# Optimization experiments

Hardware: AMD Instinct MI355X
Metric: run time of the kernel (lower is better)

## Reference

```python
import jax, jax.numpy as jnp
import numpy as np

N = 100000
E = 1600000
NFEAT = 256
NHID = 128
LATENT = 64


def setup_inputs() -> dict:
    key = jax.random.key(0)
    ks = jax.random.split(key, 12)
    x = jax.random.normal(ks[0], (N, NFEAT), dtype=jnp.float32)
    edge_index = jax.random.randint(ks[1], (2, E), 0, N, dtype=jnp.int32)
    edge_weight = jax.random.uniform(ks[2], (E,), dtype=jnp.float32)
    # GraphConvolution params: uniform(-stdv, stdv), stdv = 1/sqrt(out_features)
    s1 = 1.0 / np.sqrt(NHID)
    gc1_w = jax.random.uniform(ks[3], (NFEAT, NHID), minval=-s1, maxval=s1, dtype=jnp.float32)
    gc1_b = jax.random.uniform(ks[4], (NHID,), minval=-s1, maxval=s1, dtype=jnp.float32)
    gc2_w = jax.random.uniform(ks[5], (NHID, NHID), minval=-s1, maxval=s1, dtype=jnp.float32)
    gc2_b = jax.random.uniform(ks[6], (NHID,), minval=-s1, maxval=s1, dtype=jnp.float32)
    # nn.Linear default init: uniform(-1/sqrt(fan_in), 1/sqrt(fan_in))
    s2 = 1.0 / np.sqrt(NHID)
    mu_w = jax.random.uniform(ks[7], (NHID, LATENT), minval=-s2, maxval=s2, dtype=jnp.float32)
    mu_b = jax.random.uniform(ks[8], (LATENT,), minval=-s2, maxval=s2, dtype=jnp.float32)
    lv_w = jax.random.uniform(ks[9], (NHID, LATENT), minval=-s2, maxval=s2, dtype=jnp.float32)
    lv_b = jax.random.uniform(ks[10], (LATENT,), minval=-s2, maxval=s2, dtype=jnp.float32)
    return {"x": x, "edge_index": edge_index, "edge_weight": edge_weight,
            "gc1_w": gc1_w, "gc1_b": gc1_b, "gc2_w": gc2_w, "gc2_b": gc2_b,
            "mu_w": mu_w, "mu_b": mu_b, "lv_w": lv_w, "lv_b": lv_b}


def _spmm(edge_index, edge_weight, support):
    # out[row] += w * support[col]  (sparse adj @ dense support)
    row, col = edge_index[0], edge_index[1]
    msgs = support[col] * edge_weight[:, None]          # [E, F]
    return jax.ops.segment_sum(msgs, row, num_segments=N)


def reference(x, edge_index, edge_weight, gc1_w, gc1_b, gc2_w, gc2_b,
              mu_w, mu_b, lv_w, lv_b):
    # gc1: mm -> spmm -> bias -> relu (dropout is identity in eval mode)
    h = jax.nn.relu(_spmm(edge_index, edge_weight, x @ gc1_w) + gc1_b)
    h = jax.nn.relu(_spmm(edge_index, edge_weight, h @ gc2_w) + gc2_b)
    mu = h @ mu_w + mu_b
    log_var = h @ lv_w + lv_b
    return mu, log_var
```

## Files before the change

kernel.cpp:

```cpp
#include <hip/hip_runtime.h>
#include <hip/hip_fp16.h>

#define N_NODES 100000
#define N_EDGES 1600000
#define NFEAT   256
#define NHID    128
#define LATENT  64

#define NBUCKET 782
#define NBLKH   196
#define CHUNK   8192
#define NHIST   (NBUCKET * NBLKH)
#define NHISTT  300

typedef __attribute__((ext_vector_type(8))) short s16x8;
typedef __attribute__((ext_vector_type(4))) float f32x4;

__device__ __forceinline__ unsigned short f2bf(float f) {
    union { float f; unsigned u; } v; v.f = f;
    unsigned r = v.u + 0x7fffu + ((v.u >> 16) & 1u);
    return (unsigned short)(r >> 16);
}
__device__ __forceinline__ float bf2f(unsigned short s) {
    union { unsigned u; float f; } v; v.u = ((unsigned)s) << 16;
    return v.f;
}
__device__ __forceinline__ float bflo(unsigned u) {
    union { unsigned x; float f; } v; v.x = u << 16; return v.f;
}
__device__ __forceinline__ float bfhi(unsigned u) {
    union { unsigned x; float f; } v; v.x = u & 0xffff0000u; return v.f;
}
__device__ __forceinline__ float w15_decode(unsigned pv) {
    return __half2float(__ushort_as_half((unsigned short)(pv & 0x7fffu)));
}

__device__ __forceinline__ int incl_scan512(int v, int t, int (&s)[2][512]) {
    s[0][t] = v;
    __syncthreads();
    int p = 0;
    for (int off = 1; off < 512; off <<= 1) {
        int x = s[p][t];
        if (t >= off) x += s[p][t - off];
        s[p ^ 1][t] = x;
        p ^= 1;
        __syncthreads();
    }
    return s[p][t];
}


__device__ __forceinline__ void prep_body(
    int c, int K, int Ntot, int ncol0, int ldb0, int ldb1,
    const float* __restrict__ B0, const float* __restrict__ B1,
    unsigned short* __restrict__ out)
{
    int K8 = K >> 3;
    int total = (Ntot >> 4) * K8 * 16;
    if (c >= total) return;
    int m  = c & 15;
    int kc = (c >> 4) % K8;
    int nt = (c >> 4) / K8;
    int col = nt * 16 + m;
    const float* src; int ld, cc;
    if (col < ncol0) { src = B0; ld = ldb0; cc = col; }
    else             { src = B1; ld = ldb1; cc = col - ncol0; }
    s16x8 v;
    #pragma unroll
    for (int j = 0; j < 8; ++j)
        v[j] = (short)f2bf(src[(size_t)(kc * 8 + j) * ld + cc]);
    *(s16x8*)&out[(size_t)c * 8] = v;
}


__global__ __launch_bounds__(256) void k_pre(
    const int* __restrict__ rows, int* __restrict__ histG,
    const float* __restrict__ gc1_w, unsigned short* __restrict__ w1p,
    const float* __restrict__ gc2_w, unsigned short* __restrict__ w2p,
    const float* __restrict__ mu_w, const float* __restrict__ lv_w,
    unsigned short* __restrict__ w3p)
{
    int b = blockIdx.x;
    int t = threadIdx.x;
    if (b < NBLKH) {
        __shared__ int hist[NBUCKET];
        for (int i = t; i < NBUCKET; i += 256) hist[i] = 0;
        __syncthreads();
        int base = b * CHUNK;
        #pragma unroll 4
        for (int i = 0; i < CHUNK / 256; ++i) {
            int e = base + i * 256 + t;
            if (e < N_EDGES) {
                int r = rows[e];
                atomicAdd(&hist[r >> 7], 1);
            }
        }
        __syncthreads();
        for (int i = t; i < NBUCKET; i += 256)
            histG[(size_t)i * NBLKH + b] = hist[i];
    } else if (b < NBLKH + 16) {
        prep_body((b - NBLKH) * 256 + t, NFEAT, NHID, NHID, NHID, NHID, gc1_w, gc1_w, w1p);
    } else if (b < NBLKH + 24) {
        prep_body((b - NBLKH - 16) * 256 + t, NHID, NHID, NHID, NHID, NHID, gc2_w, gc2_w, w2p);
    } else {
        prep_body((b - NBLKH - 24) * 256 + t, NHID, NHID, LATENT, LATENT, LATENT, mu_w, lv_w, w3p);
    }
}


__global__ __launch_bounds__(512) void k_scanA(
    const int* __restrict__ histG, int* __restrict__ hist_excl,
    int* __restrict__ hbsum)
{
    __shared__ int s[2][512];
    int b = blockIdx.x, t = threadIdx.x;
    int i = b * 512 + t;
    int v = (i < NHIST) ? histG[i] : 0;
    int incl = incl_scan512(v, t, s);
    if (i < NHIST) hist_excl[i] = incl - v;
    if (t == 511) hbsum[b] = incl;
}

__global__ __launch_bounds__(512) void k_scanC(
    const int* __restrict__ hist_excl, const int* __restrict__ hbsum,
    int* __restrict__ scanned)
{
    __shared__ int s[2][512];
    __shared__ int sbase;
    int b = blockIdx.x, t = threadIdx.x;
    int v = (t < NHISTT) ? hbsum[t] : 0;
    int incl = incl_scan512(v, t, s);
    if (t == b) sbase = incl - v;
    __syncthreads();
    int base = sbase;
    int i = b * 512 + t;
    if (i < NHIST) scanned[i] = hist_excl[i] + base;
}


__global__ __launch_bounds__(256) void k_scatterA(
    const int* __restrict__ rows, const int* __restrict__ cols,
    const float* __restrict__ ew, const int* __restrict__ scanned,
    uint2* __restrict__ tmp)
{
    __shared__ int cur[NBUCKET];
    int b = blockIdx.x, t = threadIdx.x;
    for (int i = t; i < NBUCKET; i += 256)
        cur[i] = scanned[(size_t)i * NBLKH + b];
    __syncthreads();
    int base = b * CHUNK;
    #pragma unroll 4
    for (int i = 0; i < CHUNK / 256; ++i) {
        int e = base + i * 256 + t;
        if (e < N_EDGES) {
            int r = rows[e];
            unsigned hv = (unsigned)__half_as_ushort(__float2half(ew[e]));
            unsigned pv = ((unsigned)cols[e] << 15) | (hv & 0x7fffu);
            int p = atomicAdd(&cur[r >> 7], 1);
            tmp[p] = make_uint2(pv, (unsigned)r);
        }
    }
}


__global__ __launch_bounds__(256) void k_passB(
    const int* __restrict__ scanned, const uint2* __restrict__ tmp,
    unsigned* __restrict__ ecw, int* __restrict__ row_ptr)
{
    __shared__ int cnt[128];
    __shared__ int sc[2][128];
    __shared__ int cur[128];
    int b  = blockIdx.x;
    int t  = threadIdx.x;
    int r0 = b * 128;
    int beg = scanned[(size_t)b * NBLKH];
    int end = (b + 1 < NBUCKET) ? scanned[(size_t)(b + 1) * NBLKH] : N_EDGES;
    if (t < 128) cnt[t] = 0;
    __syncthreads();
    for (int e = beg + t; e < end; e += 256)
        atomicAdd(&cnt[tmp[e].y & 127], 1);
    __syncthreads();
    int p = 0;
    if (t < 128) sc[0][t] = cnt[t];
    __syncthreads();
    for (int off = 1; off < 128; off <<= 1) {
        if (t < 128) {
            int x = sc[p][t];
            if (t >= off) x += sc[p][t - off];
            sc[p ^ 1][t] = x;
        }
        p ^= 1;
        __syncthreads();
    }
    if (t < 128) {
        int excl = sc[p][t] - cnt[t];
        int rr = r0 + t;
        if (rr < N_NODES) row_ptr[rr] = beg + excl;
        cur[t] = beg + excl;
    }
    if (b == NBUCKET - 1 && t == 0) row_ptr[N_NODES] = N_EDGES;
    __syncthreads();
    for (int e = beg + t; e < end; e += 256) {
        uint2 v = tmp[e];
        int pos = atomicAdd(&cur[v.y & 127], 1);
        ecw[pos] = v.x;
    }
}


template<int AMODE, int OMODE>
__global__ __launch_bounds__(256) void k_gemm(
    int K, const float* __restrict__ A32, const unsigned short* __restrict__ A16,
    const unsigned short* __restrict__ Bpre,
    unsigned short* __restrict__ C16,
    float* __restrict__ C0, float* __restrict__ C1,
    const float* __restrict__ bias0, const float* __restrict__ bias1)
{
    __shared__ unsigned short As[2048];
    __shared__ unsigned short Bs[8192];

    const int t    = threadIdx.x;
    const int m0   = blockIdx.x * 32;
    const int lane = t & 63;
    const int w    = t >> 6;
    const int rt   = w & 1;
    const int ntb  = (w >> 1) * 4;
    const int fm   = lane & 15;
    const int q    = lane >> 4;
    const int K8   = K >> 3;

    f32x4 acc[4] = {};

    for (int kt = 0; kt < K; kt += 64) {
        {
            int r = t >> 3, kc = t & 7;
            int lo = ((r >> 4) * 8 + kc) * 128 + (r & 15) * 8;
            if (AMODE == 0) {
                const float* g = A32 + (size_t)(m0 + r) * K + kt + kc * 8;
                float4 a = *(const float4*)g;
                float4 b = *(const float4*)(g + 4);
                s16x8 v;
                v[0] = (short)f2bf(a.x); v[1] = (short)f2bf(a.y);
                v[2] = (short)f2bf(a.z); v[3] = (short)f2bf(a.w);
                v[4] = (short)f2bf(b.x); v[5] = (short)f2bf(b.y);
                v[6] = (short)f2bf(b.z); v[7] = (short)f2bf(b.w);
                *(s16x8*)&As[lo] = v;
            } else {
                const unsigned short* g = A16 + (size_t)(m0 + r) * 128 + kt + kc * 8;
                *(s16x8*)&As[lo] = *(const s16x8*)g;
            }
        }
        {
            int ktc = kt >> 3;
            #pragma unroll
            for (int i = 0; i < 4; ++i) {
                int c  = t + i * 256;
                int nt = c >> 7, kc = (c >> 4) & 7, m = c & 15;
                const unsigned short* g =
                    Bpre + ((size_t)(nt * K8 + ktc + kc) * 16 + m) * 8;
                *(s16x8*)&Bs[c * 8] = *(const s16x8*)g;
            }
        }
        __syncthreads();
        #pragma unroll
        for (int kk = 0; kk < 2; ++kk) {
            int kcq = kk * 4 + q;
            s16x8 a = *(const s16x8*)&As[(rt * 8 + kcq) * 128 + fm * 8];
            #pragma unroll
            for (int i = 0; i < 4; ++i) {
                s16x8 b = *(const s16x8*)&Bs[((ntb + i) * 8 + kcq) * 128 + fm * 8];
                acc[i] = __builtin_amdgcn_mfma_f32_16x16x32_bf16(a, b, acc[i], 0, 0, 0);
            }
        }
        __syncthreads();
    }

    #pragma unroll
    for (int i = 0; i < 4; ++i) {
        int col = (ntb + i) * 16 + fm;
        #pragma unroll
        for (int j = 0; j < 4; ++j) {
            int r = m0 + rt * 16 + q * 4 + j;
            float v = acc[i][j];
            if (OMODE == 0) {
                C16[(size_t)r * 128 + col] = f2bf(v);
            } else {
                if (col < 64) C0[(size_t)r * 64 + col]      = v + bias0[col];
                else          C1[(size_t)r * 64 + col - 64] = v + bias1[col - 64];
            }
        }
    }
}


#define EDGE4(qq, vv, aa0, aa1, aa2, aa3)                \
    {                                                    \
        float ww = w15_decode(qq);                       \
        aa0 += ww * bflo(vv.x);                          \
        aa1 += ww * bfhi(vv.x);                          \
        aa2 += ww * bflo(vv.y);                          \
        aa3 += ww * bfhi(vv.y);                          \
    }

__global__ __launch_bounds__(256) void k_spmm(const int* __restrict__ row_ptr,
                                              const unsigned* __restrict__ ecw,
                                              const unsigned short* __restrict__ sup,
                                              const float* __restrict__ bias,
                                              unsigned short* __restrict__ out) {
    int wave = threadIdx.x >> 6;
    int lane = threadIdx.x & 63;
    int row  = blockIdx.x * 4 + wave;
    if (row >= N_NODES) return;
    int half = lane >> 5;
    int fl   = lane & 31;

    int beg = row_ptr[row];
    int end = row_ptr[row + 1];
    float a0 = 0.f, a1 = 0.f, a2 = 0.f, a3 = 0.f;
    float b0 = 0.f, b1 = 0.f, b2 = 0.f, b3 = 0.f;

    int e = beg;
    for (; e + 16 <= end; e += 16) {
        unsigned q0 = ecw[e + 0 + half];
        unsigned q1 = ecw[e + 2 + half];
        unsigned q2 = ecw[e + 4 + half];
        unsigned q3 = ecw[e + 6 + half];
        unsigned q4 = ecw[e + 8 + half];
        unsigned q5 = ecw[e + 10 + half];
        unsigned q6 = ecw[e + 12 + half];
        unsigned q7 = ecw[e + 14 + half];
        uint2 v0 = *(const uint2*)(sup + (size_t)(q0 >> 15) * NHID + fl * 4);
        uint2 v1 = *(const uint2*)(sup + (size_t)(q1 >> 15) * NHID + fl * 4);
        uint2 v2 = *(const uint2*)(sup + (size_t)(q2 >> 15) * NHID + fl * 4);
        uint2 v3 = *(const uint2*)(sup + (size_t)(q3 >> 15) * NHID + fl * 4);
        uint2 v4 = *(const uint2*)(sup + (size_t)(q4 >> 15) * NHID + fl * 4);
        uint2 v5 = *(const uint2*)(sup + (size_t)(q5 >> 15) * NHID + fl * 4);
        uint2 v6 = *(const uint2*)(sup + (size_t)(q6 >> 15) * NHID + fl * 4);
        uint2 v7 = *(const uint2*)(sup + (size_t)(q7 >> 15) * NHID + fl * 4);
        EDGE4(q0, v0, a0, a1, a2, a3)
        EDGE4(q1, v1, b0, b1, b2, b3)
        EDGE4(q2, v2, a0, a1, a2, a3)
        EDGE4(q3, v3, b0, b1, b2, b3)
        EDGE4(q4, v4, a0, a1, a2, a3)
        EDGE4(q5, v5, b0, b1, b2, b3)
        EDGE4(q6, v6, a0, a1, a2, a3)
        EDGE4(q7, v7, b0, b1, b2, b3)
    }
    for (; e + 8 <= end; e += 8) {
        unsigned q0 = ecw[e + 0 + half];
        unsigned q1 = ecw[e + 2 + half];
        unsigned q2 = ecw[e + 4 + half];
        unsigned q3 = ecw[e + 6 + half];
        uint2 v0 = *(const uint2*)(sup + (size_t)(q0 >> 15) * NHID + fl * 4);
        uint2 v1 = *(const uint2*)(sup + (size_t)(q1 >> 15) * NHID + fl * 4);
        uint2 v2 = *(const uint2*)(sup + (size_t)(q2 >> 15) * NHID + fl * 4);
        uint2 v3 = *(const uint2*)(sup + (size_t)(q3 >> 15) * NHID + fl * 4);
        EDGE4(q0, v0, a0, a1, a2, a3)
        EDGE4(q1, v1, b0, b1, b2, b3)
        EDGE4(q2, v2, a0, a1, a2, a3)
        EDGE4(q3, v3, b0, b1, b2, b3)
    }
    if (e < end) {
        int last = end - 1;
        int e0 = e + 0 + half, e1 = e + 2 + half;
        int e2 = e + 4 + half, e3 = e + 6 + half;
        unsigned q0 = ecw[e0 <= last ? e0 : last];
        unsigned q1 = ecw[e1 <= last ? e1 : last];
        unsigned q2 = ecw[e2 <= last ? e2 : last];
        unsigned q3 = ecw[e3 <= last ? e3 : last];
        uint2 v0 = *(const uint2*)(sup + (size_t)(q0 >> 15) * NHID + fl * 4);
        uint2 v1 = *(const uint2*)(sup + (size_t)(q1 >> 15) * NHID + fl * 4);
        uint2 v2 = *(const uint2*)(sup + (size_t)(q2 >> 15) * NHID + fl * 4);
        uint2 v3 = *(const uint2*)(sup + (size_t)(q3 >> 15) * NHID + fl * 4);
        float w0 = (e0 <= last) ? w15_decode(q0) : 0.f;
        float w1 = (e1 <= last) ? w15_decode(q1) : 0.f;
        float w2 = (e2 <= last) ? w15_decode(q2) : 0.f;
        float w3 = (e3 <= last) ? w15_decode(q3) : 0.f;
        a0 += w0 * bflo(v0.x); a1 += w0 * bfhi(v0.x);
        a2 += w0 * bflo(v0.y); a3 += w0 * bfhi(v0.y);
        b0 += w1 * bflo(v1.x); b1 += w1 * bfhi(v1.x);
        b2 += w1 * bflo(v1.y); b3 += w1 * bfhi(v1.y);
        a0 += w2 * bflo(v2.x); a1 += w2 * bfhi(v2.x);
        a2 += w2 * bflo(v2.y); a3 += w2 * bfhi(v2.y);
        b0 += w3 * bflo(v3.x); b1 += w3 * bfhi(v3.x);
        b2 += w3 * bflo(v3.y); b3 += w3 * bfhi(v3.y);
    }

    a0 += b0; a1 += b1; a2 += b2; a3 += b3;
    a0 += __shfl_xor(a0, 32, 64);
    a1 += __shfl_xor(a1, 32, 64);
    a2 += __shfl_xor(a2, 32, 64);
    a3 += __shfl_xor(a3, 32, 64);

    if (half == 0) {
        float o0 = a0 + bias[fl * 4 + 0];
        float o1 = a1 + bias[fl * 4 + 1];
        float o2 = a2 + bias[fl * 4 + 2];
        float o3 = a3 + bias[fl * 4 + 3];
        o0 = o0 > 0.f ? o0 : 0.f;
        o1 = o1 > 0.f ? o1 : 0.f;
        o2 = o2 > 0.f ? o2 : 0.f;
        o3 = o3 > 0.f ? o3 : 0.f;
        uint2 pv;
        pv.x = (unsigned)f2bf(o0) | ((unsigned)f2bf(o1) << 16);
        pv.y = (unsigned)f2bf(o2) | ((unsigned)f2bf(o3) << 16);
        *(uint2*)(out + (size_t)row * NHID + fl * 4) = pv;
    }
}


extern "C" void kernel_launch(void* const* d_in, const int* in_sizes, int n_in,
                              void* d_out, int out_size, void* d_ws, size_t ws_size,
                              hipStream_t stream) {
    const float* x     = (const float*)d_in[0];
    const int*   ei    = (const int*)  d_in[1];
    const float* ew    = (const float*)d_in[2];
    const float* gc1_w = (const float*)d_in[3];
    const float* gc1_b = (const float*)d_in[4];
    const float* gc2_w = (const float*)d_in[5];
    const float* gc2_b = (const float*)d_in[6];
    const float* mu_w  = (const float*)d_in[7];
    const float* mu_b  = (const float*)d_in[8];
    const float* lv_w  = (const float*)d_in[9];
    const float* lv_b  = (const float*)d_in[10];
    float* out = (float*)d_out;

    const int* rows = ei;
    const int* cols = ei + N_EDGES;

    char* p = (char*)d_ws;
    auto alloc = [&](size_t bytes) {
        char* r = p;
        p += (bytes + 255) & ~(size_t)255;
        return r;
    };
    int*      row_ptr   = (int*)     alloc((size_t)(N_NODES + 1) * 4);
    int*      histG     = (int*)     alloc((size_t)NHIST * 4);
    int*      hist_excl = (int*)     alloc((size_t)NHIST * 4);
    int*      hbsum     = (int*)     alloc((size_t)NHISTT * 4);
    int*      scanned   = (int*)     alloc((size_t)NHIST * 4);
    unsigned* ecw       = (unsigned*)alloc((size_t)N_EDGES * 4);
    uint2*    tmp       = (uint2*)   alloc((size_t)N_EDGES * 8);
    unsigned short* w1p    = (unsigned short*)alloc((size_t)NFEAT * NHID * 2);
    unsigned short* w2p    = (unsigned short*)alloc((size_t)NHID * NHID * 2);
    unsigned short* w3p    = (unsigned short*)alloc((size_t)NHID * NHID * 2);
    unsigned short* bufSup = (unsigned short*)alloc((size_t)N_NODES * NHID * 2);
    unsigned short* bufH   = (unsigned short*)alloc((size_t)N_NODES * NHID * 2);
    (void)ws_size; (void)n_in; (void)in_sizes; (void)out_size;

    k_pre<<<NBLKH + 32, 256, 0, stream>>>(rows, histG,
                                          gc1_w, w1p, gc2_w, w2p, mu_w, lv_w, w3p);
    k_scanA<<<NHISTT, 512, 0, stream>>>(histG, hist_excl, hbsum);
    k_scanC<<<NHISTT, 512, 0, stream>>>(hist_excl, hbsum, scanned);
    k_scatterA<<<NBLKH, 256, 0, stream>>>(rows, cols, ew, scanned, tmp);
    k_passB<<<NBUCKET, 256, 0, stream>>>(scanned, tmp, ecw, row_ptr);

    k_gemm<0, 0><<<N_NODES / 32, 256, 0, stream>>>(NFEAT, x, nullptr, w1p,
                                                   bufSup, nullptr, nullptr, nullptr, nullptr);
    k_spmm<<<N_NODES / 4, 256, 0, stream>>>(row_ptr, ecw, bufSup, gc1_b, bufH);
    k_gemm<1, 0><<<N_NODES / 32, 256, 0, stream>>>(NHID, nullptr, bufH, w2p,
                                                   bufSup, nullptr, nullptr, nullptr, nullptr);
    k_spmm<<<N_NODES / 4, 256, 0, stream>>>(row_ptr, ecw, bufSup, gc2_b, bufH);
    k_gemm<1, 1><<<N_NODES / 32, 256, 0, stream>>>(NHID, nullptr, bufH, w3p,
                                                   nullptr, out, out + (size_t)N_NODES * LATENT,
                                                   mu_b, lv_b);
}
```

Measured before the change: 418.4 us.

## Fuse first GEMM with histogram prep and merge scan into scatter kernel

The first dense GEMM (x @ gc1_w) now runs inside the same launch as the edge histogram and weight packing. It reads gc1_w directly in fp32 and converts to bf16 on the fly instead of using a pre-packed copy. The second-level scan is folded into the scatter kernel, removing one launch and the scanned array. The temporary edge buffer shrinks from 8 bytes to 5 bytes per edge by storing the row index as a byte. The aim is fewer launches, overlap of the graph-preprocessing work with the GEMM, and less scatter traffic, at the cost of strided fp32 B loads in the GEMM and redundant scans in every scatter block.

```diff
diff --git a/kernel.cpp b/kernel.cpp
--- a/kernel.cpp
+++ b/kernel.cpp
@@ -13,6 +13,12 @@
 #define NHIST   (NBUCKET * NBLKH)
 #define NHISTT  300
 
+#define NGEMM1B 3125
+#define FR_HIST NGEMM1B
+#define FR_W2   (FR_HIST + NBLKH)
+#define FR_W3   (FR_W2 + 8)
+#define FR_TOT  (FR_W3 + 8)
+
 typedef __attribute__((ext_vector_type(8))) short s16x8;
 typedef __attribute__((ext_vector_type(4))) float f32x4;
 
@@ -20,10 +26,6 @@
     union { float f; unsigned u; } v; v.f = f;
     unsigned r = v.u + 0x7fffu + ((v.u >> 16) & 1u);
     return (unsigned short)(r >> 16);
-}
-__device__ __forceinline__ float bf2f(unsigned short s) {
-    union { unsigned u; float f; } v; v.u = ((unsigned)s) << 16;
-    return v.f;
 }
 __device__ __forceinline__ float bflo(unsigned u) {
     union { unsigned x; float f; } v; v.x = u << 16; return v.f;
@@ -73,145 +75,11 @@
 }
 
 
-__global__ __launch_bounds__(256) void k_pre(
-    const int* __restrict__ rows, int* __restrict__ histG,
-    const float* __restrict__ gc1_w, unsigned short* __restrict__ w1p,
-    const float* __restrict__ gc2_w, unsigned short* __restrict__ w2p,
-    const float* __restrict__ mu_w, const float* __restrict__ lv_w,
-    unsigned short* __restrict__ w3p)
-{
-    int b = blockIdx.x;
-    int t = threadIdx.x;
-    if (b < NBLKH) {
-        __shared__ int hist[NBUCKET];
-        for (int i = t; i < NBUCKET; i += 256) hist[i] = 0;
-        __syncthreads();
-        int base = b * CHUNK;
-        #pragma unroll 4
-        for (int i = 0; i < CHUNK / 256; ++i) {
-            int e = base + i * 256 + t;
-            if (e < N_EDGES) {
-                int r = rows[e];
-                atomicAdd(&hist[r >> 7], 1);
-            }
-        }
-        __syncthreads();
-        for (int i = t; i < NBUCKET; i += 256)
-            histG[(size_t)i * NBLKH + b] = hist[i];
-    } else if (b < NBLKH + 16) {
-        prep_body((b - NBLKH) * 256 + t, NFEAT, NHID, NHID, NHID, NHID, gc1_w, gc1_w, w1p);
-    } else if (b < NBLKH + 24) {
-        prep_body((b - NBLKH - 16) * 256 + t, NHID, NHID, NHID, NHID, NHID, gc2_w, gc2_w, w2p);
-    } else {
-        prep_body((b - NBLKH - 24) * 256 + t, NHID, NHID, LATENT, LATENT, LATENT, mu_w, lv_w, w3p);
-    }
-}
-
-
-__global__ __launch_bounds__(512) void k_scanA(
-    const int* __restrict__ histG, int* __restrict__ hist_excl,
-    int* __restrict__ hbsum)
-{
-    __shared__ int s[2][512];
-    int b = blockIdx.x, t = threadIdx.x;
-    int i = b * 512 + t;
-    int v = (i < NHIST) ? histG[i] : 0;
-    int incl = incl_scan512(v, t, s);
-    if (i < NHIST) hist_excl[i] = incl - v;
-    if (t == 511) hbsum[b] = incl;
-}
-
-__global__ __launch_bounds__(512) void k_scanC(
-    const int* __restrict__ hist_excl, const int* __restrict__ hbsum,
-    int* __restrict__ scanned)
-{
-    __shared__ int s[2][512];
-    __shared__ int sbase;
-    int b = blockIdx.x, t = threadIdx.x;
-    int v = (t < NHISTT) ? hbsum[t] : 0;
-    int incl = incl_scan512(v, t, s);
-    if (t == b) sbase = incl - v;
-    __syncthreads();
-    int base = sbase;
-    int i = b * 512 + t;
-    if (i < NHIST) scanned[i] = hist_excl[i] + base;
-}
-
-
-__global__ __launch_bounds__(256) void k_scatterA(
-    const int* __restrict__ rows, const int* __restrict__ cols,
-    const float* __restrict__ ew, const int* __restrict__ scanned,
-    uint2* __restrict__ tmp)
-{
-    __shared__ int cur[NBUCKET];
-    int b = blockIdx.x, t = threadIdx.x;
-    for (int i = t; i < NBUCKET; i += 256)
-        cur[i] = scanned[(size_t)i * NBLKH + b];
-    __syncthreads();
-    int base = b * CHUNK;
-    #pragma unroll 4
-    for (int i = 0; i < CHUNK / 256; ++i) {
-        int e = base + i * 256 + t;
-        if (e < N_EDGES) {
-            int r = rows[e];
-            unsigned hv = (unsigned)__half_as_ushort(__float2half(ew[e]));
-            unsigned pv = ((unsigned)cols[e] << 15) | (hv & 0x7fffu);
-            int p = atomicAdd(&cur[r >> 7], 1);
-            tmp[p] = make_uint2(pv, (unsigned)r);
-        }
-    }
-}
-
-
-__global__ __launch_bounds__(256) void k_passB(
-    const int* __restrict__ scanned, const uint2* __restrict__ tmp,
-    unsigned* __restrict__ ecw, int* __restrict__ row_ptr)
-{
-    __shared__ int cnt[128];
-    __shared__ int sc[2][128];
-    __shared__ int cur[128];
-    int b  = blockIdx.x;
-    int t  = threadIdx.x;
-    int r0 = b * 128;
-    int beg = scanned[(size_t)b * NBLKH];
-    int end = (b + 1 < NBUCKET) ? scanned[(size_t)(b + 1) * NBLKH] : N_EDGES;
-    if (t < 128) cnt[t] = 0;
-    __syncthreads();
-    for (int e = beg + t; e < end; e += 256)
-        atomicAdd(&cnt[tmp[e].y & 127], 1);
-    __syncthreads();
-    int p = 0;
-    if (t < 128) sc[0][t] = cnt[t];
-    __syncthreads();
-    for (int off = 1; off < 128; off <<= 1) {
-        if (t < 128) {
-            int x = sc[p][t];
-            if (t >= off) x += sc[p][t - off];
-            sc[p ^ 1][t] = x;
-        }
-        p ^= 1;
-        __syncthreads();
-    }
-    if (t < 128) {
-        int excl = sc[p][t] - cnt[t];
-        int rr = r0 + t;
-        if (rr < N_NODES) row_ptr[rr] = beg + excl;
-        cur[t] = beg + excl;
-    }
-    if (b == NBUCKET - 1 && t == 0) row_ptr[N_NODES] = N_EDGES;
-    __syncthreads();
-    for (int e = beg + t; e < end; e += 256) {
-        uint2 v = tmp[e];
-        int pos = atomicAdd(&cur[v.y & 127], 1);
-        ecw[pos] = v.x;
-    }
-}
-
-
-template<int AMODE, int OMODE>
-__global__ __launch_bounds__(256) void k_gemm(
-    int K, const float* __restrict__ A32, const unsigned short* __restrict__ A16,
-    const unsigned short* __restrict__ Bpre,
+template<int AMODE, int BMODE, int OMODE>
+__device__ __forceinline__ void gemm_body(
+    int bm, int t, int K,
+    const float* __restrict__ A32, const unsigned short* __restrict__ A16,
+    const unsigned short* __restrict__ Bpre, const float* __restrict__ Bf32,
     unsigned short* __restrict__ C16,
     float* __restrict__ C0, float* __restrict__ C1,
     const float* __restrict__ bias0, const float* __restrict__ bias1)
@@ -219,8 +87,7 @@
     __shared__ unsigned short As[2048];
     __shared__ unsigned short Bs[8192];
 
-    const int t    = threadIdx.x;
-    const int m0   = blockIdx.x * 32;
+    const int m0   = bm * 32;
     const int lane = t & 63;
     const int w    = t >> 6;
     const int rt   = w & 1;
@@ -256,9 +123,19 @@
             for (int i = 0; i < 4; ++i) {
                 int c  = t + i * 256;
                 int nt = c >> 7, kc = (c >> 4) & 7, m = c & 15;
-                const unsigned short* g =
-                    Bpre + ((size_t)(nt * K8 + ktc + kc) * 16 + m) * 8;
-                *(s16x8*)&Bs[c * 8] = *(const s16x8*)g;
+                if (BMODE == 1) {
+                    const unsigned short* g =
+                        Bpre + ((size_t)(nt * K8 + ktc + kc) * 16 + m) * 8;
+                    *(s16x8*)&Bs[c * 8] = *(const s16x8*)g;
+                } else {
+                    int col = nt * 16 + m;
+                    const float* g = Bf32 + (size_t)(kt + kc * 8) * 128 + col;
+                    s16x8 v;
+                    #pragma unroll
+                    for (int j = 0; j < 8; ++j)
+                        v[j] = (short)f2bf(g[(size_t)j * 128]);
+                    *(s16x8*)&Bs[c * 8] = v;
+                }
             }
         }
         __syncthreads();
@@ -290,6 +167,155 @@
             }
         }
     }
+}
+
+
+__global__ __launch_bounds__(256) void k_front(
+    const float* __restrict__ x, const int* __restrict__ rows,
+    int* __restrict__ histG,
+    const float* __restrict__ gc1_w, unsigned short* __restrict__ bufSup,
+    const float* __restrict__ gc2_w, unsigned short* __restrict__ w2p,
+    const float* __restrict__ mu_w, const float* __restrict__ lv_w,
+    unsigned short* __restrict__ w3p)
+{
+    int b = blockIdx.x;
+    int t = threadIdx.x;
+    if (b < NGEMM1B) {
+        gemm_body<0, 0, 0>(b, t, NFEAT, x, nullptr, nullptr, gc1_w,
+                           bufSup, nullptr, nullptr, nullptr, nullptr);
+    } else if (b < FR_W2) {
+        __shared__ int hist[NBUCKET];
+        int hb = b - FR_HIST;
+        for (int i = t; i < NBUCKET; i += 256) hist[i] = 0;
+        __syncthreads();
+        int base = hb * CHUNK;
+        #pragma unroll 4
+        for (int i = 0; i < CHUNK / 256; ++i) {
+            int e = base + i * 256 + t;
+            if (e < N_EDGES) {
+                int r = rows[e];
+                atomicAdd(&hist[r >> 7], 1);
+            }
+        }
+        __syncthreads();
+        for (int i = t; i < NBUCKET; i += 256)
+            histG[(size_t)i * NBLKH + hb] = hist[i];
+    } else if (b < FR_W3) {
+        prep_body((b - FR_W2) * 256 + t, NHID, NHID, NHID, NHID, NHID, gc2_w, gc2_w, w2p);
+    } else {
+        prep_body((b - FR_W3) * 256 + t, NHID, NHID, LATENT, LATENT, LATENT, mu_w, lv_w, w3p);
+    }
+}
+
+
+__global__ __launch_bounds__(512) void k_scanA(
+    const int* __restrict__ histG, int* __restrict__ hist_excl,
+    int* __restrict__ hbsum)
+{
+    __shared__ int s[2][512];
+    int b = blockIdx.x, t = threadIdx.x;
+    int i = b * 512 + t;
+    int v = (i < NHIST) ? histG[i] : 0;
+    int incl = incl_scan512(v, t, s);
+    if (i < NHIST) hist_excl[i] = incl - v;
+    if (t == 511) hbsum[b] = incl;
+}
+
+
+__global__ __launch_bounds__(512) void k_scatterA(
+    const int* __restrict__ rows, const int* __restrict__ cols,
+    const float* __restrict__ ew,
+    const int* __restrict__ hist_excl, const int* __restrict__ hbsum,
+    unsigned* __restrict__ tmp_pv, unsigned char* __restrict__ tmp_row,
+    int* __restrict__ bucket_start)
+{
+    __shared__ int s[2][512];
+    __shared__ int tbase[NHISTT];
+    __shared__ int cur[NBUCKET];
+    int b = blockIdx.x, t = threadIdx.x;
+    int v = (t < NHISTT) ? hbsum[t] : 0;
+    int incl = incl_scan512(v, t, s);
+    if (t < NHISTT) tbase[t] = incl - v;
+    __syncthreads();
+    for (int i = t; i < NBUCKET; i += 512) {
+        int idx = i * NBLKH + b;
+        int val = hist_excl[idx] + tbase[idx >> 9];
+        cur[i] = val;
+        if (b == 0) bucket_start[i] = val;
+    }
+    __syncthreads();
+    int base = b * CHUNK;
+    #pragma unroll 4
+    for (int i = 0; i < CHUNK / 512; ++i) {
+        int e = base + i * 512 + t;
+        if (e < N_EDGES) {
+            int r = rows[e];
+            unsigned hv = (unsigned)__half_as_ushort(__float2half(ew[e]));
+            unsigned pv = ((unsigned)cols[e] << 15) | (hv & 0x7fffu);
+            int p = atomicAdd(&cur[r >> 7], 1);
+            tmp_pv[p]  = pv;
+            tmp_row[p] = (unsigned char)(r & 127);
+        }
+    }
+}
+
+
+__global__ __launch_bounds__(256) void k_passB(
+    const int* __restrict__ bucket_start, const unsigned* __restrict__ tmp_pv,
+    const unsigned char* __restrict__ tmp_row,
+    unsigned* __restrict__ ecw, int* __restrict__ row_ptr)
+{
+    __shared__ int cnt[128];
+    __shared__ int sc[2][128];
+    __shared__ int cur[128];
+    int b  = blockIdx.x;
+    int t  = threadIdx.x;
+    int r0 = b * 128;
+    int beg = bucket_start[b];
+    int end = (b + 1 < NBUCKET) ? bucket_start[b + 1] : N_EDGES;
+    if (t < 128) cnt[t] = 0;
+    __syncthreads();
+    for (int e = beg + t; e < end; e += 256)
+        atomicAdd(&cnt[tmp_row[e]], 1);
+    __syncthreads();
+    int p = 0;
+    if (t < 128) sc[0][t] = cnt[t];
+    __syncthreads();
+    for (int off = 1; off < 128; off <<= 1) {
+        if (t < 128) {
+            int x = sc[p][t];
+            if (t >= off) x += sc[p][t - off];
+            sc[p ^ 1][t] = x;
+        }
+        p ^= 1;
+        __syncthreads();
+    }
+    if (t < 128) {
+        int excl = sc[p][t] - cnt[t];
+        int rr = r0 + t;
+        if (rr < N_NODES) row_ptr[rr] = beg + excl;
+        cur[t] = beg + excl;
+    }
+    if (b == NBUCKET - 1 && t == 0) row_ptr[N_NODES] = N_EDGES;
+    __syncthreads();
+    for (int e = beg + t; e < end; e += 256) {
+        unsigned pv = tmp_pv[e];
+        int pos = atomicAdd(&cur[tmp_row[e]], 1);
+        ecw[pos] = pv;
+    }
+}
+
+
+template<int AMODE, int OMODE>
+__global__ __launch_bounds__(256) void k_gemm(
+    int K, const float* __restrict__ A32, const unsigned short* __restrict__ A16,
+    const unsigned short* __restrict__ Bpre,
+    unsigned short* __restrict__ C16,
+    float* __restrict__ C0, float* __restrict__ C1,
+    const float* __restrict__ bias0, const float* __restrict__ bias1)
+{
+    gemm_body<AMODE, 1, OMODE>(blockIdx.x, threadIdx.x, K, A32, A16, Bpre,
+                               nullptr, C16, C0, C1, bias0, bias1);
 }
 
 
@@ -434,29 +460,27 @@
         p += (bytes + 255) & ~(size_t)255;
         return r;
     };
-    int*      row_ptr   = (int*)     alloc((size_t)(N_NODES + 1) * 4);
-    int*      histG     = (int*)     alloc((size_t)NHIST * 4);
-    int*      hist_excl = (int*)     alloc((size_t)NHIST * 4);
-    int*      hbsum     = (int*)     alloc((size_t)NHISTT * 4);
-    int*      scanned   = (int*)     alloc((size_t)NHIST * 4);
-    unsigned* ecw       = (unsigned*)alloc((size_t)N_EDGES * 4);
-    uint2*    tmp       = (uint2*)   alloc((size_t)N_EDGES * 8);
-    unsigned short* w1p    = (unsigned short*)alloc((size_t)NFEAT * NHID * 2);
+    int*      row_ptr      = (int*)     alloc((size_t)(N_NODES + 1) * 4);
+    int*      histG        = (int*)     alloc((size_t)NHIST * 4);
+    int*      hist_excl    = (int*)     alloc((size_t)NHIST * 4);
+    int*      hbsum        = (int*)     alloc((size_t)NHISTT * 4);
+    int*      bucket_start = (int*)     alloc((size_t)NBUCKET * 4);
+    unsigned* ecw          = (unsigned*)alloc((size_t)N_EDGES * 4);
+    unsigned* tmp_pv       = (unsigned*)alloc((size_t)N_EDGES * 4);
+    unsigned char* tmp_row = (unsigned char*)alloc((size_t)N_EDGES);
     unsigned short* w2p    = (unsigned short*)alloc((size_t)NHID * NHID * 2);
     unsigned short* w3p    = (unsigned short*)alloc((size_t)NHID * NHID * 2);
     unsigned short* bufSup = (unsigned short*)alloc((size_t)N_NODES * NHID * 2);
     unsigned short* bufH   = (unsigned short*)alloc((size_t)N_NODES * NHID * 2);
     (void)ws_size; (void)n_in; (void)in_sizes; (void)out_size;
 
-    k_pre<<<NBLKH + 32, 256, 0, stream>>>(rows, histG,
-                                          gc1_w, w1p, gc2_w, w2p, mu_w, lv_w, w3p);
+    k_front<<<FR_TOT, 256, 0, stream>>>(x, rows, histG, gc1_w, bufSup,
+                                        gc2_w, w2p, mu_w, lv_w, w3p);
     k_scanA<<<NHISTT, 512, 0, stream>>>(histG, hist_excl, hbsum);
-    k_scanC<<<NHISTT, 512, 0, stream>>>(hist_excl, hbsum, scanned);
-    k_scatterA<<<NBLKH, 256, 0, stream>>>(rows, cols, ew, scanned, tmp);
-    k_passB<<<NBUCKET, 256, 0, stream>>>(scanned, tmp, ecw, row_ptr);
-
-    k_gemm<0, 0><<<N_NODES / 32, 256, 0, stream>>>(NFEAT, x, nullptr, w1p,
-                                                   bufSup, nullptr, nullptr, nullptr, nullptr);
+    k_scatterA<<<NBLKH, 512, 0, stream>>>(rows, cols, ew, hist_excl, hbsum,
+                                          tmp_pv, tmp_row, bucket_start);
+    k_passB<<<NBUCKET, 256, 0, stream>>>(bucket_start, tmp_pv, tmp_row, ecw, row_ptr);
+
     k_spmm<<<N_NODES / 4, 256, 0, stream>>>(row_ptr, ecw, bufSup, gc1_b, bufH);
     k_gemm<1, 0><<<N_NODES / 32, 256, 0, stream>>>(NHID, nullptr, bufH, w2p,
                                                    bufSup, nullptr, nullptr, nullptr, nullptr);
```

Measured after the change: 438.9 us. +4.9%, slower.
